# Kernel optimization log

Measured on AMD Instinct MI355X. Metric: run time of the kernel, lower is better.

## Reference

```python
import jax, jax.numpy as jnp
import numpy as np

B, L, D = 2, 2048, 512
H, HD = 8, 64          # num_heads, head_dim (hidden_dim = 512)
WINDOW = 256
SCALE = float(np.sqrt(HD))
LN_EPS = 1e-5


def setup_inputs() -> dict:
    key = jax.random.key(0)
    ks = jax.random.split(key, 10)
    sequence = jax.random.normal(ks[0], (B, L, D), dtype=jnp.float32)
    # lengths in [L - WINDOW//2, L] so no query row is fully masked (avoids NaN, matches original's valid regime)
    sequence_lengths = jax.random.randint(ks[1], (B,), L - WINDOW // 2, L + 1, dtype=jnp.int32)
    timestamps = jnp.sort(jax.random.uniform(ks[2], (B, L), dtype=jnp.float32) * float(L), axis=-1)
    w_std = 0.02
    Wq = jax.random.normal(ks[3], (H * HD, D), dtype=jnp.float32) * w_std
    Wk = jax.random.normal(ks[4], (H * HD, D), dtype=jnp.float32) * w_std
    Wv = jax.random.normal(ks[5], (H * HD, D), dtype=jnp.float32) * w_std
    Wo = jax.random.normal(ks[6], (D, H * HD), dtype=jnp.float32) * w_std
    bo = jnp.zeros((D,), dtype=jnp.float32)
    ln_gamma = jnp.ones((D,), dtype=jnp.float32)
    ln_beta = jnp.zeros((D,), dtype=jnp.float32)
    temporal_weight = jnp.array([0.1], dtype=jnp.float32)
    return {
        "sequence": sequence, "sequence_lengths": sequence_lengths, "timestamps": timestamps,
        "ln_gamma": ln_gamma, "ln_beta": ln_beta,
        "Wq": Wq, "Wk": Wk, "Wv": Wv, "Wo": Wo, "bo": bo,
        "temporal_weight": temporal_weight,
    }


def reference(sequence, sequence_lengths, timestamps, ln_gamma, ln_beta,
              Wq, Wk, Wv, Wo, bo, temporal_weight):
    residual = sequence
    # LayerNorm over input_dim
    mu = jnp.mean(sequence, axis=-1, keepdims=True)
    var = jnp.mean(jnp.square(sequence - mu), axis=-1, keepdims=True)
    x = (sequence - mu) * jax.lax.rsqrt(var + LN_EPS) * ln_gamma + ln_beta

    # QKV projections (spectral-normalized Linear, no bias) -> [B, L, H, HD]
    Q = (x @ Wq.T).reshape(B, L, H, HD)
    K = (x @ Wk.T).reshape(B, L, H, HD)
    V = (x @ Wv.T).reshape(B, L, H, HD)

    scores = jnp.einsum("bqhd,bkhd->bhqk", Q, K) / SCALE  # [B, H, L, L]

    # temporal decay bias
    ts_diff = jnp.abs(timestamps[:, :, None] - timestamps[:, None, :])  # [B, L, L]
    temporal_weights = jnp.exp(-jnp.abs(temporal_weight[0]) * ts_diff)
    scores = scores + jnp.log(temporal_weights + 1e-8)[:, None, :, :]

    neg_inf = jnp.float32(-jnp.inf)
    # sliding window mask (L > window_size): |i - j| <= window_size // 2
    idx = jnp.arange(L)
    wmask = jnp.abs(idx[None, :] - idx[:, None]) <= WINDOW // 2  # [L, L]
    scores = jnp.where(wmask[None, None, :, :], scores, neg_inf)

    # padding mask on key positions
    pmask = idx[None, :] < sequence_lengths[:, None]  # [B, L]
    scores = jnp.where(pmask[:, None, None, :], scores, neg_inf)

    attn = jax.nn.softmax(scores, axis=-1)  # [B, H, L, L]
    attended = jnp.einsum("bhqk,bkhd->bqhd", attn, V).reshape(B, L, H * HD)

    output = attended @ Wo.T + bo + residual  # [B, L, D]

    # exponential position-weighted aggregation over valid positions
    pos = idx.astype(jnp.float32)
    pw = jnp.exp(-0.1 * (L - 1 - pos))[None, :] * pmask.astype(jnp.float32)  # [B, L]
    pw = pw / (jnp.sum(pw, axis=1, keepdims=True) + 1e-8)
    aggregated = jnp.sum(output * pw[:, :, None], axis=1)  # [B, D]
    return aggregated
```

## Files before the change

### kernel.cpp

```cpp
#include <hip/hip_runtime.h>
#include <math.h>

#define B 2
#define L 2048
#define D 512
#define H 8
#define HD 64
#define W2 128
#define NOUT (3*D)

#define QS 1792
#define NQ (L - QS)
#define ROWS0 (QS - W2)
#define NROWS (L - ROWS0)
#define MROWS (B * NROWS)

#define TQ 8
#define NQT (NQ / TQ)

typedef __bf16 bf16_t;
typedef __attribute__((ext_vector_type(4))) __bf16 bf16x4;
typedef __attribute__((ext_vector_type(8))) __bf16 bf16x8;
typedef __attribute__((ext_vector_type(4))) float f32x4;

#define PREP_LN_BLOCKS (MROWS / 4)
#define PREP_CVT_BLOCKS 768
#define PREP_AGGS_BLOCKS 64
#define PREP_GRID (PREP_LN_BLOCKS + PREP_CVT_BLOCKS + PREP_AGGS_BLOCKS + 1)

__global__ __launch_bounds__(256) void prep_kernel(const float* __restrict__ seq,
                                                   const float* __restrict__ gamma,
                                                   const float* __restrict__ beta,
                                                   const float* __restrict__ Wq,
                                                   const float* __restrict__ Wk,
                                                   const float* __restrict__ Wv,
                                                   const int* __restrict__ slen,
                                                   bf16_t* __restrict__ xb,
                                                   bf16_t* __restrict__ wb,
                                                   float* __restrict__ aggA,
                                                   float* __restrict__ aggSp) {
    int blk = blockIdx.x;
    int tid = threadIdx.x;
    int wid = tid >> 6, lane = tid & 63;

    if (blk < PREP_LN_BLOCKS) {
        int row = blk * 4 + wid;
        int b = row / NROWS;
        int l = ROWS0 + (row - b * NROWS);
        const float* src = seq + ((size_t)b * L + l) * D;
        float4 v0 = ((const float4*)src)[lane];
        float4 v1 = ((const float4*)src)[lane + 64];
        float s  = v0.x + v0.y + v0.z + v0.w + v1.x + v1.y + v1.z + v1.w;
        float sq = v0.x*v0.x + v0.y*v0.y + v0.z*v0.z + v0.w*v0.w
                 + v1.x*v1.x + v1.y*v1.y + v1.z*v1.z + v1.w*v1.w;
        for (int o = 32; o; o >>= 1) { s += __shfl_xor(s, o); sq += __shfl_xor(sq, o); }
        float mu = s * (1.0f / D);
        float var = sq * (1.0f / D) - mu * mu;
        float rstd = rsqrtf(var + 1e-5f);
        float4 g0 = ((const float4*)gamma)[lane];
        float4 g1 = ((const float4*)gamma)[lane + 64];
        float4 b0 = ((const float4*)beta)[lane];
        float4 b1 = ((const float4*)beta)[lane + 64];
        bf16x4 c0, c1;
        c0[0] = (bf16_t)((v0.x - mu) * rstd * g0.x + b0.x);
        c0[1] = (bf16_t)((v0.y - mu) * rstd * g0.y + b0.y);
        c0[2] = (bf16_t)((v0.z - mu) * rstd * g0.z + b0.z);
        c0[3] = (bf16_t)((v0.w - mu) * rstd * g0.w + b0.w);
        c1[0] = (bf16_t)((v1.x - mu) * rstd * g1.x + b1.x);
        c1[1] = (bf16_t)((v1.y - mu) * rstd * g1.y + b1.y);
        c1[2] = (bf16_t)((v1.z - mu) * rstd * g1.z + b1.z);
        c1[3] = (bf16_t)((v1.w - mu) * rstd * g1.w + b1.w);
        bf16x4* dst = (bf16x4*)(xb + (size_t)row * D);
        dst[lane] = c0;
        dst[lane + 64] = c1;
    } else if (blk < PREP_LN_BLOCKS + PREP_CVT_BLOCKS) {
        int idx = (blk - PREP_LN_BLOCKS) * 256 + tid;
        const float* src = (idx < 65536) ? Wq : (idx < 131072 ? Wk : Wv);
        int off = idx & 65535;
        float4 v = ((const float4*)src)[off];
        bf16x4 o;
        o[0] = (bf16_t)v.x; o[1] = (bf16_t)v.y; o[2] = (bf16_t)v.z; o[3] = (bf16_t)v.w;
        ((bf16x4*)wb)[idx] = o;
    } else if (blk < PREP_LN_BLOCKS + PREP_CVT_BLOCKS + PREP_AGGS_BLOCKS) {
        __shared__ float red[4][64];
        int idx = blk - (PREP_LN_BLOCKS + PREP_CVT_BLOCKS);
        int b = idx >> 5;
        int rc = (idx >> 3) & 3;
        int ct = idx & 7;
        int col = ct * 64 + lane;
        int nv = slen[b] - QS;
        int i0 = rc * 64 + wid * 16;
        int i1 = min(i0 + 16, nv);
        float s2 = 0.f;
#pragma unroll 4
        for (int i = i0; i < i1; ++i) {
            s2 += __expf(-0.1f * (float)(NQ - 1 - i)) * seq[((size_t)(b * L + QS + i)) * D + col];
        }
        red[wid][lane] = s2;
        __syncthreads();
        if (wid == 0) {
            aggSp[(size_t)rc * (B * D) + b * D + col] =
                red[0][lane] + red[1][lane] + red[2][lane] + red[3][lane];
        }
    } else {
        ((float4*)aggA)[tid] = make_float4(0.f, 0.f, 0.f, 0.f);
    }
}

__global__ __launch_bounds__(256) void qkv_gemm(const bf16_t* __restrict__ xb,
                                                const bf16_t* __restrict__ wb,
                                                bf16_t* __restrict__ Qb,
                                                bf16_t* __restrict__ Kb,
                                                bf16_t* __restrict__ Vb) {
    int m0 = blockIdx.x * 32, n0 = blockIdx.y * 64;
    int wid = threadIdx.x >> 6, lane = threadIdx.x & 63;
    int mw = m0 + (wid >> 1) * 16;
    int nw = n0 + (wid & 1) * 32;
    int mr = lane & 15, quad = lane >> 4;
    f32x4 acc0 = {}, acc1 = {};
    const bf16_t* aptr = xb + (size_t)(mw + mr) * D + quad * 8;
    const bf16_t* bptr = wb + (size_t)(nw + mr) * D + quad * 8;
#pragma unroll 8
    for (int k = 0; k < D; k += 32) {
        bf16x8 a  = *(const bf16x8*)(aptr + k);
        bf16x8 b0 = *(const bf16x8*)(bptr + k);
        bf16x8 b1 = *(const bf16x8*)(bptr + 16 * D + k);
        acc0 = __builtin_amdgcn_mfma_f32_16x16x32_bf16(a, b0, acc0, 0, 0, 0);
        acc1 = __builtin_amdgcn_mfma_f32_16x16x32_bf16(a, b1, acc1, 0, 0, 0);
    }
    int sec = n0 >> 9;
    int h = (n0 >> 6) & 7;
    int d0 = nw & 63;
    bf16_t* dstbase = (sec == 0) ? Qb : (sec == 1 ? Kb : Vb);
    int m = mw + quad * 4;
    int b = m / NROWS;
    int r = m - b * NROWS;
    bf16_t* dst = dstbase + ((size_t)(b * H + h) * NROWS + r) * HD + d0 + mr;
#pragma unroll
    for (int rr = 0; rr < 4; ++rr) {
        dst[(size_t)rr * HD]      = (bf16_t)acc0[rr];
        dst[(size_t)rr * HD + 16] = (bf16_t)acc1[rr];
    }
}

__global__ __launch_bounds__(256) void attn_kernel(const bf16_t* __restrict__ Qb,
                                                   const bf16_t* __restrict__ Kb,
                                                   const bf16_t* __restrict__ Vb,
                                                   const float* __restrict__ ts,
                                                   const int* __restrict__ slen,
                                                   const float* __restrict__ tw,
                                                   float* __restrict__ aggA) {
    int bid = blockIdx.x;
    int b = bid / (NQT * H);
    int rem = bid - b * (NQT * H);
    int qt = rem / H;
    int h = rem - qt * H;
    int wid = threadIdx.x >> 6;
    int lane = threadIdx.x & 63;
    int q0 = QS + qt * TQ;
    int sl = slen[b];
    if (q0 >= sl) return;
    int kmin = q0 - W2;
    int kmax = min(q0 + TQ - 1 + W2, sl - 1);
    int nk = kmax - kmin + 1;
    int chunk = (nk + 3) >> 2;
    int start = wid * chunk;
    int end = min(start + chunk, nk);
    int cnt = max(end - start, 0);

    __shared__ __attribute__((aligned(16))) float qv[TQ][HD];
    __shared__ __attribute__((aligned(16))) float p[4][66][TQ];
    __shared__ __attribute__((aligned(16))) float pacc[4][TQ][HD];
    __shared__ float mlm[4][TQ];
    __shared__ float mll[4][TQ];
    __shared__ float tqs[TQ];

    const size_t headbase = (size_t)(b * H + h) * NROWS;

    {
        int qr = q0 + wid - ROWS0;
        qv[wid][lane]     = (float)Qb[(headbase + qr) * HD + lane];
        qv[wid + 4][lane] = (float)Qb[(headbase + qr + 4) * HD + lane];
        if (threadIdx.x < TQ) tqs[threadIdx.x] = ts[b * L + q0 + threadIdx.x];
    }
    __syncthreads();

    float atw = fabsf(tw[0]);

    float m[TQ], sreg[2][TQ];
#pragma unroll
    for (int t = 0; t < TQ; ++t) m[t] = -INFINITY;
#pragma unroll
    for (int it = 0; it < 2; ++it) {
        int kk = start + it * 64 + lane;
        bool act = (kk < end);
        float s[TQ];
#pragma unroll
        for (int t = 0; t < TQ; ++t) s[t] = 0.f;
        if (act) {
            int k = kmin + kk;
            const bf16_t* Krow = Kb + (headbase + (k - ROWS0)) * HD;
#pragma unroll
            for (int d8 = 0; d8 < 8; ++d8) {
                bf16x8 kv = *(const bf16x8*)(Krow + d8 * 8);
                float kf0 = (float)kv[0], kf1 = (float)kv[1], kf2 = (float)kv[2], kf3 = (float)kv[3];
                float kf4 = (float)kv[4], kf5 = (float)kv[5], kf6 = (float)kv[6], kf7 = (float)kv[7];
#pragma unroll
                for (int t = 0; t < TQ; ++t) {
                    const float* qq = &qv[t][d8 * 8];
                    s[t] += qq[0]*kf0 + qq[1]*kf1 + qq[2]*kf2 + qq[3]*kf3
                          + qq[4]*kf4 + qq[5]*kf5 + qq[6]*kf6 + qq[7]*kf7;
                }
            }
            float tk = ts[b * L + k];
#pragma unroll
            for (int t = 0; t < TQ; ++t) {
                float dt = fabsf(tqs[t] - tk);
                float bias = __logf(__expf(-atw * dt) + 1e-8f);
                int qa = q0 + t;
                bool valid = (k >= qa - W2) && (k <= qa + W2);
                s[t] = valid ? (s[t] * 0.125f + bias) : -INFINITY;
            }
        } else {
#pragma unroll
            for (int t = 0; t < TQ; ++t) s[t] = -INFINITY;
        }
#pragma unroll
        for (int t = 0; t < TQ; ++t) { sreg[it][t] = s[t]; m[t] = fmaxf(m[t], s[t]); }
    }
#pragma unroll
    for (int t = 0; t < TQ; ++t)
        for (int o = 32; o; o >>= 1) m[t] = fmaxf(m[t], __shfl_xor(m[t], o));

    float l[TQ];
#pragma unroll
    for (int t = 0; t < TQ; ++t) l[t] = 0.f;
#pragma unroll
    for (int it = 0; it < 2; ++it) {
        int kk = start + it * 64 + lane;
        bool act = (kk < end);
        float pv[TQ];
#pragma unroll
        for (int t = 0; t < TQ; ++t) {
            float pp = (m[t] > -INFINITY) ? __expf(sreg[it][t] - m[t]) : 0.0f;
            pv[t] = pp;
            l[t] += act ? pp : 0.0f;
        }
        if (act) {
            *(float4*)&p[wid][kk - start][0] = make_float4(pv[0], pv[1], pv[2], pv[3]);
            *(float4*)&p[wid][kk - start][4] = make_float4(pv[4], pv[5], pv[6], pv[7]);
        }
    }
#pragma unroll
    for (int t = 0; t < TQ; ++t)
        for (int o = 32; o; o >>= 1) l[t] += __shfl_xor(l[t], o);
    if (lane == 0) {
#pragma unroll
        for (int t = 0; t < TQ; ++t) { mlm[wid][t] = m[t]; mll[wid][t] = l[t]; }
    }

    float acc[TQ];
#pragma unroll
    for (int t = 0; t < TQ; ++t) acc[t] = 0.f;
    const bf16_t* Vbase = Vb + (headbase + (kmin + start - ROWS0)) * HD + lane;
#pragma unroll 4
    for (int kl = 0; kl < cnt; ++kl) {
        float v = (float)Vbase[(size_t)kl * HD];
        float4 p0 = *(const float4*)&p[wid][kl][0];
        float4 p1 = *(const float4*)&p[wid][kl][4];
        acc[0] += p0.x * v; acc[1] += p0.y * v; acc[2] += p0.z * v; acc[3] += p0.w * v;
        acc[4] += p1.x * v; acc[5] += p1.y * v; acc[6] += p1.z * v; acc[7] += p1.w * v;
    }
#pragma unroll
    for (int t = 0; t < TQ; ++t) pacc[wid][t][lane] = acc[t];
    __syncthreads();

#pragma unroll
    for (int half = 0; half < 2; ++half) {
        int t = wid + half * 4;
        int q = q0 + t;
        if (q < sl) {
            float m0 = mlm[0][t], m1 = mlm[1][t], m2 = mlm[2][t], m3 = mlm[3][t];
            float M = fmaxf(fmaxf(m0, m1), fmaxf(m2, m3));
            float e0 = __expf(m0 - M), e1 = __expf(m1 - M), e2 = __expf(m2 - M), e3 = __expf(m3 - M);
            float Lsum = e0 * mll[0][t] + e1 * mll[1][t] + e2 * mll[2][t] + e3 * mll[3][t];
            float o = e0 * pacc[0][t][lane] + e1 * pacc[1][t][lane]
                    + e2 * pacc[2][t][lane] + e3 * pacc[3][t][lane];
            float wq = __expf(-0.1f * (float)(L - 1 - q));
            atomicAdd(&aggA[b * D + h * HD + lane], (o / Lsum) * wq);
        }
    }
}

__global__ __launch_bounds__(64) void out_kernel(const float* __restrict__ aggA,
                                                 const float* __restrict__ aggSp,
                                                 const float* __restrict__ Wo,
                                                 const float* __restrict__ bo,
                                                 const int* __restrict__ slen,
                                                 float* __restrict__ out) {
    int d = blockIdx.x;
    int lane = threadIdx.x;
    int nv0 = slen[0] - QS, nv1 = slen[1] - QS;
    float den0 = 0.f, den1 = 0.f;
#pragma unroll
    for (int j = 0; j < 4; ++j) {
        int i = lane * 4 + j;
        float w = __expf(-0.1f * (float)(NQ - 1 - i));
        den0 += (i < nv0) ? w : 0.0f;
        den1 += (i < nv1) ? w : 0.0f;
    }
    for (int o = 32; o; o >>= 1) { den0 += __shfl_xor(den0, o); den1 += __shfl_xor(den1, o); }

    const float* wrow = Wo + (size_t)d * D;
    float acc0 = 0.0f, acc1 = 0.0f;
#pragma unroll
    for (int i = 0; i < 8; ++i) {
        int j = lane + 64 * i;
        float w = wrow[j];
        acc0 += aggA[j] * w;
        acc1 += aggA[D + j] * w;
    }
    for (int o = 32; o; o >>= 1) { acc0 += __shfl_xor(acc0, o); acc1 += __shfl_xor(acc1, o); }
    if (lane == 0) {
        float s0 = aggSp[d]         + aggSp[B*D + d]         + aggSp[2*B*D + d]         + aggSp[3*B*D + d];
        float s1 = aggSp[D + d]     + aggSp[B*D + D + d]     + aggSp[2*B*D + D + d]     + aggSp[3*B*D + D + d];
        out[d]     = (acc0 + s0 + bo[d] * den0) / (den0 + 1e-8f);
        out[D + d] = (acc1 + s1 + bo[d] * den1) / (den1 + 1e-8f);
    }
}

extern "C" void kernel_launch(void* const* d_in, const int* in_sizes, int n_in,
                              void* d_out, int out_size, void* d_ws, size_t ws_size,
                              hipStream_t stream) {
    const float* seq   = (const float*)d_in[0];
    const int*   slen  = (const int*)d_in[1];
    const float* ts    = (const float*)d_in[2];
    const float* gamma = (const float*)d_in[3];
    const float* beta  = (const float*)d_in[4];
    const float* Wq    = (const float*)d_in[5];
    const float* Wk    = (const float*)d_in[6];
    const float* Wv    = (const float*)d_in[7];
    const float* Wo    = (const float*)d_in[8];
    const float* bo    = (const float*)d_in[9];
    const float* tw    = (const float*)d_in[10];
    float* out = (float*)d_out;

    float* ws    = (float*)d_ws;
    float* aggA  = ws;
    float* aggSp = aggA + B * D;
    bf16_t* xb   = (bf16_t*)(aggSp + 4 * B * D);
    bf16_t* wb   = xb + (size_t)MROWS * D;
    bf16_t* Qb   = wb + (size_t)NOUT * D;
    bf16_t* Kb   = Qb + (size_t)B * H * NROWS * HD;
    bf16_t* Vb   = Kb + (size_t)B * H * NROWS * HD;

    prep_kernel<<<PREP_GRID, 256, 0, stream>>>(seq, gamma, beta, Wq, Wk, Wv, slen,
                                               xb, wb, aggA, aggSp);
    dim3 ggrid(MROWS / 32, NOUT / 64);
    qkv_gemm<<<ggrid, 256, 0, stream>>>(xb, wb, Qb, Kb, Vb);
    attn_kernel<<<B * NQT * H, 256, 0, stream>>>(Qb, Kb, Vb, ts, slen, tw, aggA);
    out_kernel<<<D, 64, 0, stream>>>(aggA, aggSp, Wo, bo, slen, out);
}
```

Measured before the change: 122.6 us.

## Fuse LayerNorm and fp32 weight conversion into the QKV GEMM kernel

Merges the prep kernel and the QKV GEMM into one launch. Each GEMM block recomputes LayerNorm for its 32 rows into shared memory and converts the fp32 weights to bf16 in registers while loading them. This drops one kernel launch and the global round trip of the bf16 activation and weight buffers. In exchange, LayerNorm is recomputed once per N-tile (24 times per row) and every block re-reads and re-converts fp32 weights, which doubles the weight bytes loaded. The attention block-index division is also replaced with shifts.

```diff
diff --git a/kernel.cpp b/kernel.cpp
--- a/kernel.cpp
+++ b/kernel.cpp
@@ -23,67 +23,105 @@
 typedef __attribute__((ext_vector_type(8))) __bf16 bf16x8;
 typedef __attribute__((ext_vector_type(4))) float f32x4;
 
-#define PREP_LN_BLOCKS (MROWS / 4)
-#define PREP_CVT_BLOCKS 768
-#define PREP_AGGS_BLOCKS 64
-#define PREP_GRID (PREP_LN_BLOCKS + PREP_CVT_BLOCKS + PREP_AGGS_BLOCKS + 1)
-
-__global__ __launch_bounds__(256) void prep_kernel(const float* __restrict__ seq,
-                                                   const float* __restrict__ gamma,
-                                                   const float* __restrict__ beta,
-                                                   const float* __restrict__ Wq,
-                                                   const float* __restrict__ Wk,
-                                                   const float* __restrict__ Wv,
-                                                   const int* __restrict__ slen,
-                                                   bf16_t* __restrict__ xb,
-                                                   bf16_t* __restrict__ wb,
-                                                   float* __restrict__ aggA,
-                                                   float* __restrict__ aggSp) {
+#define G_GEMM 576
+#define G_AGGS 64
+#define G_TOTAL (G_GEMM + G_AGGS + 1)
+
+#define XS_STR 520
+
+__global__ __launch_bounds__(256) void gemm_fused(const float* __restrict__ seq,
+                                                  const float* __restrict__ gamma,
+                                                  const float* __restrict__ beta,
+                                                  const float* __restrict__ Wq,
+                                                  const float* __restrict__ Wk,
+                                                  const float* __restrict__ Wv,
+                                                  const int* __restrict__ slen,
+                                                  bf16_t* __restrict__ Qb,
+                                                  bf16_t* __restrict__ Kb,
+                                                  bf16_t* __restrict__ Vb,
+                                                  float* __restrict__ aggA,
+                                                  float* __restrict__ aggSp) {
+    __shared__ __attribute__((aligned(16))) bf16_t xs[32][XS_STR];
     int blk = blockIdx.x;
     int tid = threadIdx.x;
     int wid = tid >> 6, lane = tid & 63;
 
-    if (blk < PREP_LN_BLOCKS) {
-        int row = blk * 4 + wid;
-        int b = row / NROWS;
-        int l = ROWS0 + (row - b * NROWS);
-        const float* src = seq + ((size_t)b * L + l) * D;
-        float4 v0 = ((const float4*)src)[lane];
-        float4 v1 = ((const float4*)src)[lane + 64];
-        float s  = v0.x + v0.y + v0.z + v0.w + v1.x + v1.y + v1.z + v1.w;
-        float sq = v0.x*v0.x + v0.y*v0.y + v0.z*v0.z + v0.w*v0.w
-                 + v1.x*v1.x + v1.y*v1.y + v1.z*v1.z + v1.w*v1.w;
-        for (int o = 32; o; o >>= 1) { s += __shfl_xor(s, o); sq += __shfl_xor(sq, o); }
-        float mu = s * (1.0f / D);
-        float var = sq * (1.0f / D) - mu * mu;
-        float rstd = rsqrtf(var + 1e-5f);
-        float4 g0 = ((const float4*)gamma)[lane];
-        float4 g1 = ((const float4*)gamma)[lane + 64];
-        float4 b0 = ((const float4*)beta)[lane];
-        float4 b1 = ((const float4*)beta)[lane + 64];
-        bf16x4 c0, c1;
-        c0[0] = (bf16_t)((v0.x - mu) * rstd * g0.x + b0.x);
-        c0[1] = (bf16_t)((v0.y - mu) * rstd * g0.y + b0.y);
-        c0[2] = (bf16_t)((v0.z - mu) * rstd * g0.z + b0.z);
-        c0[3] = (bf16_t)((v0.w - mu) * rstd * g0.w + b0.w);
-        c1[0] = (bf16_t)((v1.x - mu) * rstd * g1.x + b1.x);
-        c1[1] = (bf16_t)((v1.y - mu) * rstd * g1.y + b1.y);
-        c1[2] = (bf16_t)((v1.z - mu) * rstd * g1.z + b1.z);
-        c1[3] = (bf16_t)((v1.w - mu) * rstd * g1.w + b1.w);
-        bf16x4* dst = (bf16x4*)(xb + (size_t)row * D);
-        dst[lane] = c0;
-        dst[lane + 64] = c1;
-    } else if (blk < PREP_LN_BLOCKS + PREP_CVT_BLOCKS) {
-        int idx = (blk - PREP_LN_BLOCKS) * 256 + tid;
-        const float* src = (idx < 65536) ? Wq : (idx < 131072 ? Wk : Wv);
-        int off = idx & 65535;
-        float4 v = ((const float4*)src)[off];
-        bf16x4 o;
-        o[0] = (bf16_t)v.x; o[1] = (bf16_t)v.y; o[2] = (bf16_t)v.z; o[3] = (bf16_t)v.w;
-        ((bf16x4*)wb)[idx] = o;
-    } else if (blk < PREP_LN_BLOCKS + PREP_CVT_BLOCKS + PREP_AGGS_BLOCKS) {
-        __shared__ float red[4][64];
-        int idx = blk - (PREP_LN_BLOCKS + PREP_CVT_BLOCKS);
+    if (blk < G_GEMM) {
+        int m0 = (blk % 24) * 32, n0 = (blk / 24) * 64;
+
+        float4 g0 = ((const float4*)gamma)[lane * 2];
+        float4 g1 = ((const float4*)gamma)[lane * 2 + 1];
+        float4 be0 = ((const float4*)beta)[lane * 2];
+        float4 be1 = ((const float4*)beta)[lane * 2 + 1];
+#pragma unroll
+        for (int j = 0; j < 8; ++j) {
+            int rl = wid * 8 + j;
+            int row = m0 + rl;
+            int b = row / NROWS;
+            int l = ROWS0 + (row - b * NROWS);
+            const float* src = seq + ((size_t)b * L + l) * D + lane * 8;
+            float4 v0 = *(const float4*)src;
+            float4 v1 = *(const float4*)(src + 4);
+            float s  = v0.x + v0.y + v0.z + v0.w + v1.x + v1.y + v1.z + v1.w;
+            float sq = v0.x*v0.x + v0.y*v0.y + v0.z*v0.z + v0.w*v0.w
+                     + v1.x*v1.x + v1.y*v1.y + v1.z*v1.z + v1.w*v1.w;
+            for (int o = 32; o; o >>= 1) { s += __shfl_xor(s, o); sq += __shfl_xor(sq, o); }
+            float mu = s * (1.0f / D);
+            float var = sq * (1.0f / D) - mu * mu;
+            float rstd = rsqrtf(var + 1e-5f);
+            bf16x8 c;
+            c[0] = (bf16_t)((v0.x - mu) * rstd * g0.x + be0.x);
+            c[1] = (bf16_t)((v0.y - mu) * rstd * g0.y + be0.y);
+            c[2] = (bf16_t)((v0.z - mu) * rstd * g0.z + be0.z);
+            c[3] = (bf16_t)((v0.w - mu) * rstd * g0.w + be0.w);
+            c[4] = (bf16_t)((v1.x - mu) * rstd * g1.x + be1.x);
+            c[5] = (bf16_t)((v1.y - mu) * rstd * g1.y + be1.y);
+            c[6] = (bf16_t)((v1.z - mu) * rstd * g1.z + be1.z);
+            c[7] = (bf16_t)((v1.w - mu) * rstd * g1.w + be1.w);
+            *(bf16x8*)&xs[rl][lane * 8] = c;
+        }
+        __syncthreads();
+
+        int sec = n0 >> 9;
+        const float* Wmat = (sec == 0) ? Wq : (sec == 1 ? Wk : Wv);
+        int mwl = (wid >> 1) * 16;
+        int nw = (wid & 1) * 32;
+        int mr = lane & 15, quad = lane >> 4;
+        int obase = (n0 & 511) + nw;
+        const float* Brow0 = Wmat + (size_t)(obase + mr) * D + quad * 8;
+        const float* Brow1 = Brow0 + (size_t)16 * D;
+        const bf16_t* arow = &xs[mwl + mr][quad * 8];
+        f32x4 acc0 = {}, acc1 = {};
+#pragma unroll 4
+        for (int k = 0; k < D; k += 32) {
+            bf16x8 a = *(const bf16x8*)(arow + k);
+            float4 f00 = *(const float4*)(Brow0 + k);
+            float4 f01 = *(const float4*)(Brow0 + k + 4);
+            float4 f10 = *(const float4*)(Brow1 + k);
+            float4 f11 = *(const float4*)(Brow1 + k + 4);
+            bf16x8 b0, b1;
+            b0[0] = (bf16_t)f00.x; b0[1] = (bf16_t)f00.y; b0[2] = (bf16_t)f00.z; b0[3] = (bf16_t)f00.w;
+            b0[4] = (bf16_t)f01.x; b0[5] = (bf16_t)f01.y; b0[6] = (bf16_t)f01.z; b0[7] = (bf16_t)f01.w;
+            b1[0] = (bf16_t)f10.x; b1[1] = (bf16_t)f10.y; b1[2] = (bf16_t)f10.z; b1[3] = (bf16_t)f10.w;
+            b1[4] = (bf16_t)f11.x; b1[5] = (bf16_t)f11.y; b1[6] = (bf16_t)f11.z; b1[7] = (bf16_t)f11.w;
+            acc0 = __builtin_amdgcn_mfma_f32_16x16x32_bf16(a, b0, acc0, 0, 0, 0);
+            acc1 = __builtin_amdgcn_mfma_f32_16x16x32_bf16(a, b1, acc1, 0, 0, 0);
+        }
+        int h = (n0 >> 6) & 7;
+        int d0 = nw & 63;
+        bf16_t* dstbase = (sec == 0) ? Qb : (sec == 1 ? Kb : Vb);
+        int m = m0 + mwl + quad * 4;
+        int b = m / NROWS;
+        int r = m - b * NROWS;
+        bf16_t* dst = dstbase + ((size_t)(b * H + h) * NROWS + r) * HD + d0 + mr;
+#pragma unroll
+        for (int rr = 0; rr < 4; ++rr) {
+            dst[(size_t)rr * HD]      = (bf16_t)acc0[rr];
+            dst[(size_t)rr * HD + 16] = (bf16_t)acc1[rr];
+        }
+    } else if (blk < G_GEMM + G_AGGS) {
+        float (*red)[64] = (float (*)[64])xs;
+        int idx = blk - G_GEMM;
         int b = idx >> 5;
         int rc = (idx >> 3) & 3;
         int ct = idx & 7;
@@ -107,42 +145,6 @@
     }
 }
 
-__global__ __launch_bounds__(256) void qkv_gemm(const bf16_t* __restrict__ xb,
-                                                const bf16_t* __restrict__ wb,
-                                                bf16_t* __restrict__ Qb,
-                                                bf16_t* __restrict__ Kb,
-                                                bf16_t* __restrict__ Vb) {
-    int m0 = blockIdx.x * 32, n0 = blockIdx.y * 64;
-    int wid = threadIdx.x >> 6, lane = threadIdx.x & 63;
-    int mw = m0 + (wid >> 1) * 16;
-    int nw = n0 + (wid & 1) * 32;
-    int mr = lane & 15, quad = lane >> 4;
-    f32x4 acc0 = {}, acc1 = {};
-    const bf16_t* aptr = xb + (size_t)(mw + mr) * D + quad * 8;
-    const bf16_t* bptr = wb + (size_t)(nw + mr) * D + quad * 8;
-#pragma unroll 8
-    for (int k = 0; k < D; k += 32) {
-        bf16x8 a  = *(const bf16x8*)(aptr + k);
-        bf16x8 b0 = *(const bf16x8*)(bptr + k);
-        bf16x8 b1 = *(const bf16x8*)(bptr + 16 * D + k);
-        acc0 = __builtin_amdgcn_mfma_f32_16x16x32_bf16(a, b0, acc0, 0, 0, 0);
-        acc1 = __builtin_amdgcn_mfma_f32_16x16x32_bf16(a, b1, acc1, 0, 0, 0);
-    }
-    int sec = n0 >> 9;
-    int h = (n0 >> 6) & 7;
-    int d0 = nw & 63;
-    bf16_t* dstbase = (sec == 0) ? Qb : (sec == 1 ? Kb : Vb);
-    int m = mw + quad * 4;
-    int b = m / NROWS;
-    int r = m - b * NROWS;
-    bf16_t* dst = dstbase + ((size_t)(b * H + h) * NROWS + r) * HD + d0 + mr;
-#pragma unroll
-    for (int rr = 0; rr < 4; ++rr) {
-        dst[(size_t)rr * HD]      = (bf16_t)acc0[rr];
-        dst[(size_t)rr * HD + 16] = (bf16_t)acc1[rr];
-    }
-}
-
 __global__ __launch_bounds__(256) void attn_kernel(const bf16_t* __restrict__ Qb,
                                                    const bf16_t* __restrict__ Kb,
                                                    const bf16_t* __restrict__ Vb,
@@ -151,10 +153,10 @@
                                                    const float* __restrict__ tw,
                                                    float* __restrict__ aggA) {
     int bid = blockIdx.x;
-    int b = bid / (NQT * H);
-    int rem = bid - b * (NQT * H);
-    int qt = rem / H;
-    int h = rem - qt * H;
+    int b = bid >> 8;
+    int rem = bid & 255;
+    int qt = rem >> 3;
+    int h = rem & 7;
     int wid = threadIdx.x >> 6;
     int lane = threadIdx.x & 63;
     int q0 = QS + qt * TQ;
@@ -322,8 +324,8 @@
     }
     for (int o = 32; o; o >>= 1) { acc0 += __shfl_xor(acc0, o); acc1 += __shfl_xor(acc1, o); }
     if (lane == 0) {
-        float s0 = aggSp[d]         + aggSp[B*D + d]         + aggSp[2*B*D + d]         + aggSp[3*B*D + d];
-        float s1 = aggSp[D + d]     + aggSp[B*D + D + d]     + aggSp[2*B*D + D + d]     + aggSp[3*B*D + D + d];
+        float s0 = aggSp[d]     + aggSp[B*D + d]     + aggSp[2*B*D + d]     + aggSp[3*B*D + d];
+        float s1 = aggSp[D + d] + aggSp[B*D + D + d] + aggSp[2*B*D + D + d] + aggSp[3*B*D + D + d];
         out[d]     = (acc0 + s0 + bo[d] * den0) / (den0 + 1e-8f);
         out[D + d] = (acc1 + s1 + bo[d] * den1) / (den1 + 1e-8f);
     }
@@ -348,16 +350,12 @@
     float* ws    = (float*)d_ws;
     float* aggA  = ws;
     float* aggSp = aggA + B * D;
-    bf16_t* xb   = (bf16_t*)(aggSp + 4 * B * D);
-    bf16_t* wb   = xb + (size_t)MROWS * D;
-    bf16_t* Qb   = wb + (size_t)NOUT * D;
+    bf16_t* Qb   = (bf16_t*)(aggSp + 4 * B * D);
     bf16_t* Kb   = Qb + (size_t)B * H * NROWS * HD;
     bf16_t* Vb   = Kb + (size_t)B * H * NROWS * HD;
 
-    prep_kernel<<<PREP_GRID, 256, 0, stream>>>(seq, gamma, beta, Wq, Wk, Wv, slen,
-                                               xb, wb, aggA, aggSp);
-    dim3 ggrid(MROWS / 32, NOUT / 64);
-    qkv_gemm<<<ggrid, 256, 0, stream>>>(xb, wb, Qb, Kb, Vb);
+    gemm_fused<<<G_TOTAL, 256, 0, stream>>>(seq, gamma, beta, Wq, Wk, Wv, slen,
+                                            Qb, Kb, Vb, aggA, aggSp);
     attn_kernel<<<B * NQT * H, 256, 0, stream>>>(Qb, Kb, Vb, ts, slen, tw, aggA);
     out_kernel<<<D, 64, 0, stream>>>(aggA, aggSp, Wo, bo, slen, out);
 }
```

After: 127.2 us. 3.8% more time.

## Fuse weight bf16 conversion into QKV GEMM and halve attention query tile

Applied to the files above, without the earlier changes.

Drops the separate fp32-to-bf16 conversion of Wq/Wk/Wv from the prep kernel. The QKV GEMM now reads fp32 weights directly and converts them in registers, which removes the extra weight write and re-read through the workspace. The attention query tile shrinks from 8 to 4 rows, doubling the block count for more parallelism. The cost is that each block reloads the same K/V window for fewer queries, and the GEMM reads twice as many weight bytes per block.

```diff
diff --git a/kernel.cpp b/kernel.cpp
--- a/kernel.cpp
+++ b/kernel.cpp
@@ -15,7 +15,7 @@
 #define NROWS (L - ROWS0)
 #define MROWS (B * NROWS)
 
-#define TQ 8
+#define TQ 4
 #define NQT (NQ / TQ)
 
 typedef __bf16 bf16_t;
@@ -24,21 +24,17 @@
 typedef __attribute__((ext_vector_type(4))) float f32x4;
 
 #define PREP_LN_BLOCKS (MROWS / 4)
-#define PREP_CVT_BLOCKS 768
 #define PREP_AGGS_BLOCKS 64
-#define PREP_GRID (PREP_LN_BLOCKS + PREP_CVT_BLOCKS + PREP_AGGS_BLOCKS + 1)
+#define PREP_GRID (PREP_LN_BLOCKS + PREP_AGGS_BLOCKS + 1)
 
 __global__ __launch_bounds__(256) void prep_kernel(const float* __restrict__ seq,
                                                    const float* __restrict__ gamma,
                                                    const float* __restrict__ beta,
-                                                   const float* __restrict__ Wq,
-                                                   const float* __restrict__ Wk,
-                                                   const float* __restrict__ Wv,
                                                    const int* __restrict__ slen,
                                                    bf16_t* __restrict__ xb,
-                                                   bf16_t* __restrict__ wb,
                                                    float* __restrict__ aggA,
                                                    float* __restrict__ aggSp) {
+    __shared__ float red[4][64];
     int blk = blockIdx.x;
     int tid = threadIdx.x;
     int wid = tid >> 6, lane = tid & 63;
@@ -73,17 +69,8 @@
         bf16x4* dst = (bf16x4*)(xb + (size_t)row * D);
         dst[lane] = c0;
         dst[lane + 64] = c1;
-    } else if (blk < PREP_LN_BLOCKS + PREP_CVT_BLOCKS) {
-        int idx = (blk - PREP_LN_BLOCKS) * 256 + tid;
-        const float* src = (idx < 65536) ? Wq : (idx < 131072 ? Wk : Wv);
-        int off = idx & 65535;
-        float4 v = ((const float4*)src)[off];
-        bf16x4 o;
-        o[0] = (bf16_t)v.x; o[1] = (bf16_t)v.y; o[2] = (bf16_t)v.z; o[3] = (bf16_t)v.w;
-        ((bf16x4*)wb)[idx] = o;
-    } else if (blk < PREP_LN_BLOCKS + PREP_CVT_BLOCKS + PREP_AGGS_BLOCKS) {
-        __shared__ float red[4][64];
-        int idx = blk - (PREP_LN_BLOCKS + PREP_CVT_BLOCKS);
+    } else if (blk < PREP_LN_BLOCKS + PREP_AGGS_BLOCKS) {
+        int idx = blk - PREP_LN_BLOCKS;
         int b = idx >> 5;
         int rc = (idx >> 3) & 3;
         int ct = idx & 7;
@@ -108,34 +95,45 @@
 }
 
 __global__ __launch_bounds__(256) void qkv_gemm(const bf16_t* __restrict__ xb,
-                                                const bf16_t* __restrict__ wb,
+                                                const float* __restrict__ Wq,
+                                                const float* __restrict__ Wk,
+                                                const float* __restrict__ Wv,
                                                 bf16_t* __restrict__ Qb,
                                                 bf16_t* __restrict__ Kb,
                                                 bf16_t* __restrict__ Vb) {
     int m0 = blockIdx.x * 32, n0 = blockIdx.y * 64;
     int wid = threadIdx.x >> 6, lane = threadIdx.x & 63;
     int mw = m0 + (wid >> 1) * 16;
-    int nw = n0 + (wid & 1) * 32;
+    int nwl = (wid & 1) * 32;
     int mr = lane & 15, quad = lane >> 4;
+    int sec = n0 >> 9;
+    const float* Wmat = (sec == 0) ? Wq : (sec == 1 ? Wk : Wv);
+    int wrow = (n0 & 511) + nwl;
     f32x4 acc0 = {}, acc1 = {};
     const bf16_t* aptr = xb + (size_t)(mw + mr) * D + quad * 8;
-    const bf16_t* bptr = wb + (size_t)(nw + mr) * D + quad * 8;
+    const float* Brow0 = Wmat + (size_t)(wrow + mr) * D + quad * 8;
+    const float* Brow1 = Brow0 + (size_t)16 * D;
 #pragma unroll 8
     for (int k = 0; k < D; k += 32) {
-        bf16x8 a  = *(const bf16x8*)(aptr + k);
-        bf16x8 b0 = *(const bf16x8*)(bptr + k);
-        bf16x8 b1 = *(const bf16x8*)(bptr + 16 * D + k);
+        bf16x8 a = *(const bf16x8*)(aptr + k);
+        float4 f00 = *(const float4*)(Brow0 + k);
+        float4 f01 = *(const float4*)(Brow0 + k + 4);
+        float4 f10 = *(const float4*)(Brow1 + k);
+        float4 f11 = *(const float4*)(Brow1 + k + 4);
+        bf16x8 b0, b1;
+        b0[0] = (bf16_t)f00.x; b0[1] = (bf16_t)f00.y; b0[2] = (bf16_t)f00.z; b0[3] = (bf16_t)f00.w;
+        b0[4] = (bf16_t)f01.x; b0[5] = (bf16_t)f01.y; b0[6] = (bf16_t)f01.z; b0[7] = (bf16_t)f01.w;
+        b1[0] = (bf16_t)f10.x; b1[1] = (bf16_t)f10.y; b1[2] = (bf16_t)f10.z; b1[3] = (bf16_t)f10.w;
+        b1[4] = (bf16_t)f11.x; b1[5] = (bf16_t)f11.y; b1[6] = (bf16_t)f11.z; b1[7] = (bf16_t)f11.w;
         acc0 = __builtin_amdgcn_mfma_f32_16x16x32_bf16(a, b0, acc0, 0, 0, 0);
         acc1 = __builtin_amdgcn_mfma_f32_16x16x32_bf16(a, b1, acc1, 0, 0, 0);
     }
-    int sec = n0 >> 9;
     int h = (n0 >> 6) & 7;
-    int d0 = nw & 63;
     bf16_t* dstbase = (sec == 0) ? Qb : (sec == 1 ? Kb : Vb);
     int m = mw + quad * 4;
     int b = m / NROWS;
     int r = m - b * NROWS;
-    bf16_t* dst = dstbase + ((size_t)(b * H + h) * NROWS + r) * HD + d0 + mr;
+    bf16_t* dst = dstbase + ((size_t)(b * H + h) * NROWS + r) * HD + nwl + mr;
 #pragma unroll
     for (int rr = 0; rr < 4; ++rr) {
         dst[(size_t)rr * HD]      = (bf16_t)acc0[rr];
@@ -179,24 +177,20 @@
 
     {
         int qr = q0 + wid - ROWS0;
-        qv[wid][lane]     = (float)Qb[(headbase + qr) * HD + lane];
-        qv[wid + 4][lane] = (float)Qb[(headbase + qr + 4) * HD + lane];
-        if (threadIdx.x < TQ) tqs[threadIdx.x] = ts[b * L + q0 + threadIdx.x];
+        qv[wid][lane] = (float)Qb[(headbase + qr) * HD + lane];
+        if (lane == 0) tqs[wid] = ts[b * L + q0 + wid];
     }
     __syncthreads();
 
     float atw = fabsf(tw[0]);
 
-    float m[TQ], sreg[2][TQ];
-#pragma unroll
-    for (int t = 0; t < TQ; ++t) m[t] = -INFINITY;
+    float m[TQ] = {-INFINITY, -INFINITY, -INFINITY, -INFINITY};
+    float sreg[2][TQ];
 #pragma unroll
     for (int it = 0; it < 2; ++it) {
         int kk = start + it * 64 + lane;
         bool act = (kk < end);
-        float s[TQ];
-#pragma unroll
-        for (int t = 0; t < TQ; ++t) s[t] = 0.f;
+        float s[TQ] = {0.f, 0.f, 0.f, 0.f};
         if (act) {
             int k = kmin + kk;
             const bf16_t* Krow = Kb + (headbase + (k - ROWS0)) * HD;
@@ -232,9 +226,7 @@
     for (int t = 0; t < TQ; ++t)
         for (int o = 32; o; o >>= 1) m[t] = fmaxf(m[t], __shfl_xor(m[t], o));
 
-    float l[TQ];
-#pragma unroll
-    for (int t = 0; t < TQ; ++t) l[t] = 0.f;
+    float l[TQ] = {0.f, 0.f, 0.f, 0.f};
 #pragma unroll
     for (int it = 0; it < 2; ++it) {
         int kk = start + it * 64 + lane;
@@ -248,7 +240,6 @@
         }
         if (act) {
             *(float4*)&p[wid][kk - start][0] = make_float4(pv[0], pv[1], pv[2], pv[3]);
-            *(float4*)&p[wid][kk - start][4] = make_float4(pv[4], pv[5], pv[6], pv[7]);
         }
     }
 #pragma unroll
@@ -259,25 +250,20 @@
         for (int t = 0; t < TQ; ++t) { mlm[wid][t] = m[t]; mll[wid][t] = l[t]; }
     }
 
-    float acc[TQ];
-#pragma unroll
-    for (int t = 0; t < TQ; ++t) acc[t] = 0.f;
+    float acc[TQ] = {0.f, 0.f, 0.f, 0.f};
     const bf16_t* Vbase = Vb + (headbase + (kmin + start - ROWS0)) * HD + lane;
 #pragma unroll 4
     for (int kl = 0; kl < cnt; ++kl) {
         float v = (float)Vbase[(size_t)kl * HD];
-        float4 p0 = *(const float4*)&p[wid][kl][0];
-        float4 p1 = *(const float4*)&p[wid][kl][4];
-        acc[0] += p0.x * v; acc[1] += p0.y * v; acc[2] += p0.z * v; acc[3] += p0.w * v;
-        acc[4] += p1.x * v; acc[5] += p1.y * v; acc[6] += p1.z * v; acc[7] += p1.w * v;
+        float4 pp = *(const float4*)&p[wid][kl][0];
+        acc[0] += pp.x * v; acc[1] += pp.y * v; acc[2] += pp.z * v; acc[3] += pp.w * v;
     }
 #pragma unroll
     for (int t = 0; t < TQ; ++t) pacc[wid][t][lane] = acc[t];
     __syncthreads();
 
-#pragma unroll
-    for (int half = 0; half < 2; ++half) {
-        int t = wid + half * 4;
+    {
+        int t = wid;
         int q = q0 + t;
         if (q < sl) {
             float m0 = mlm[0][t], m1 = mlm[1][t], m2 = mlm[2][t], m3 = mlm[3][t];
@@ -322,8 +308,8 @@
     }
     for (int o = 32; o; o >>= 1) { acc0 += __shfl_xor(acc0, o); acc1 += __shfl_xor(acc1, o); }
     if (lane == 0) {
-        float s0 = aggSp[d]         + aggSp[B*D + d]         + aggSp[2*B*D + d]         + aggSp[3*B*D + d];
-        float s1 = aggSp[D + d]     + aggSp[B*D + D + d]     + aggSp[2*B*D + D + d]     + aggSp[3*B*D + D + d];
+        float s0 = aggSp[d]     + aggSp[B*D + d]     + aggSp[2*B*D + d]     + aggSp[3*B*D + d];
+        float s1 = aggSp[D + d] + aggSp[B*D + D + d] + aggSp[2*B*D + D + d] + aggSp[3*B*D + D + d];
         out[d]     = (acc0 + s0 + bo[d] * den0) / (den0 + 1e-8f);
         out[D + d] = (acc1 + s1 + bo[d] * den1) / (den1 + 1e-8f);
     }
@@ -349,15 +335,13 @@
     float* aggA  = ws;
     float* aggSp = aggA + B * D;
     bf16_t* xb   = (bf16_t*)(aggSp + 4 * B * D);
-    bf16_t* wb   = xb + (size_t)MROWS * D;
-    bf16_t* Qb   = wb + (size_t)NOUT * D;
+    bf16_t* Qb   = xb + (size_t)MROWS * D;
     bf16_t* Kb   = Qb + (size_t)B * H * NROWS * HD;
     bf16_t* Vb   = Kb + (size_t)B * H * NROWS * HD;
 
-    prep_kernel<<<PREP_GRID, 256, 0, stream>>>(seq, gamma, beta, Wq, Wk, Wv, slen,
-                                               xb, wb, aggA, aggSp);
+    prep_kernel<<<PREP_GRID, 256, 0, stream>>>(seq, gamma, beta, slen, xb, aggA, aggSp);
     dim3 ggrid(MROWS / 32, NOUT / 64);
-    qkv_gemm<<<ggrid, 256, 0, stream>>>(xb, wb, Qb, Kb, Vb);
+    qkv_gemm<<<ggrid, 256, 0, stream>>>(xb, Wq, Wk, Wv, Qb, Kb, Vb);
     attn_kernel<<<B * NQT * H, 256, 0, stream>>>(Qb, Kb, Vb, ts, slen, tw, aggA);
     out_kernel<<<D, 64, 0, stream>>>(aggA, aggSp, Wo, bo, slen, out);
 }
```

After: 125.5 us. 2.4% more time.
